# Performance work log

Measured on AMD Instinct MI355X. Metric: run time of the kernel, lower is better.

Reference implementation:

```python
import jax, jax.numpy as jnp
import numpy as np

T, B, N, D, H = 128, 64, 24, 256, 8
F = D // H  # 32


def setup_inputs() -> dict:
    key = jax.random.key(0)
    ks = jax.random.split(key, 7)
    s = 1.0 / np.sqrt(D)  # torch nn.Linear default init range
    inputs = jax.random.normal(ks[0], (T, B, N * D), dtype=jnp.float32)
    Wk = jax.random.uniform(ks[1], (H, F, D), minval=-s, maxval=s, dtype=jnp.float32)
    bk = jax.random.uniform(ks[2], (H, F), minval=-s, maxval=s, dtype=jnp.float32)
    Wv = jax.random.uniform(ks[3], (H, F, D), minval=-s, maxval=s, dtype=jnp.float32)
    bv = jax.random.uniform(ks[4], (H, F), minval=-s, maxval=s, dtype=jnp.float32)
    Wq = jax.random.uniform(ks[5], (H, N, F, D), minval=-s, maxval=s, dtype=jnp.float32)
    bq = jax.random.uniform(ks[6], (H, N, F), minval=-s, maxval=s, dtype=jnp.float32)
    return {"inputs": inputs, "Wk": Wk, "bk": bk, "Wv": Wv, "bv": bv, "Wq": Wq, "bq": bq}


def reference(inputs, Wk, bk, Wv, bv, Wq, bq):
    # inputs: (T, B, N*D) -> (T, B, N, D)
    x = inputs.reshape(T, B, N, D)
    # shared K/V per head: (T, B, H, N, F)
    k = jnp.einsum('tbnd,hfd->tbhnf', x, Wk) + bk[:, None, :]
    v = jnp.einsum('tbnd,hfd->tbhnf', x, Wv) + bv[:, None, :]
    # per-joint Q: joint n uses its own (F, D) weight -> (T, B, H, N, F)
    q = jnp.einsum('tbnd,hnfd->tbhnf', x, Wq) + bq
    # attention over joints, scaled by sqrt(F)
    scores = jnp.einsum('tbhnf,tbhmf->tbhnm', q, k) / jnp.sqrt(jnp.float32(F))
    attn = jax.nn.softmax(scores, axis=-1)
    out = jnp.einsum('tbhnm,tbhmf->tbhnf', attn, v)
    # concat heads along feature dim per joint, then flatten joints: (T, B, N*H*F)
    out = out.transpose(0, 1, 3, 2, 4).reshape(T, B, N * H * F)
    # dropout is identity in eval mode
    return out
```

## Files before the change

kernel.cpp:

```cpp
#include <hip/hip_runtime.h>
#include <hip/hip_bf16.h>
#include <cstdio>

#define TB  8192
#define N_  24
#define D_  256
#define H_  8
#define F_  32
#define ND  6144
#define HNF 6144

typedef unsigned short u16;
typedef __attribute__((ext_vector_type(8))) _Float16 f16x8;
typedef __attribute__((ext_vector_type(8))) short bf16x8;
typedef __attribute__((ext_vector_type(4))) float f32x4;

__device__ __forceinline__ u16 f2b(float f) {
    unsigned int u = __float_as_uint(f);
    return (u16)((u + 0x7FFFu + ((u >> 16) & 1u)) >> 16);
}
__device__ __forceinline__ float b2f(u16 s) {
    return __uint_as_float(((unsigned int)s) << 16);
}
__device__ __forceinline__ u16 f2h(float f) {
    _Float16 h = (_Float16)f;
    u16 u; __builtin_memcpy(&u, &h, 2); return u;
}

__device__ __forceinline__ void gl_lds16(const void* g, void* l) {
    __builtin_amdgcn_global_load_lds(
        (const __attribute__((address_space(1))) unsigned int*)g,
        (__attribute__((address_space(3))) unsigned int*)l, 16, 0, 0);
}

__global__ __launch_bounds__(256) void prep_weights(
    const float* __restrict__ Wk, const float* __restrict__ Wv,
    const float* __restrict__ Wq, u16* __restrict__ Bp)
{
    const int idx = blockIdx.x * 256 + threadIdx.x;
    if (idx >= 24 * 8 * 48 * 64) return;
    const int fr = idx & 15;
    const int fq = (idx >> 4) & 3;
    const int g  = (idx >> 6) % 48;
    const int kt = (idx / (64 * 48)) % 8;
    const int n  = idx / (64 * 48 * 8);
    const int col = g * 16 + fr;
    const int d0  = kt * 32 + fq * 8;
    const int c   = col & 255;
    const float* src;
    if (col < 256)      src = Wk + (size_t)c * 256 + d0;
    else if (col < 512) src = Wv + (size_t)c * 256 + d0;
    else {
        const int h = c >> 5, f = c & 31;
        src = Wq + ((size_t)(h * 24 + n) * 32 + f) * 256 + d0;
    }
    __align__(16) u16 out[8];
    #pragma unroll
    for (int j = 0; j < 8; ++j) out[j] = f2h(src[j]);
    *reinterpret_cast<uint4*>(Bp + (size_t)idx * 8) =
        *reinterpret_cast<const uint4*>(out);
}

__global__ __launch_bounds__(256) void prep_bias(
    const float* __restrict__ bk, const float* __restrict__ bv,
    const float* __restrict__ bq, float* __restrict__ biasp)
{
    const int idx = blockIdx.x * 256 + threadIdx.x;
    if (idx >= 24 * 768) return;
    const int col = idx % 768, n = idx / 768;
    const int c = col & 255;
    float v;
    if (col < 256)      v = bk[c];
    else if (col < 512) v = bv[c];
    else { const int h = c >> 5, f = c & 31; v = bq[(h * 24 + n) * 32 + f]; }
    biasp[n * 768 + col] = v;
}

__global__ __launch_bounds__(512, 4) void proj_mfma(
    const float* __restrict__ x,
    const u16* __restrict__ Bp,
    const float* __restrict__ biasp,
    u16* __restrict__ kb, u16* __restrict__ vb, u16* __restrict__ qb)
{
    const int lin  = blockIdx.x;
    const int mblk = lin & 63;
    const int ct   = (lin >> 6) % 3;
    const int n    = lin / 192;
    const int tb0  = mblk * 128;
    const int tid  = threadIdx.x;
    const int w    = tid >> 6;
    const int lane = tid & 63;
    const int wm   = w >> 2;
    const int wn   = w & 3;
    const int fr   = lane & 15, fq = lane >> 4;

    __shared__ __align__(16) u16 smem[32768];
    char* Ab = (char*)smem;
    char* Bb = (char*)smem + 16384;

    const int arow0 = w * 16 + (lane >> 3);
    const int aclog = (lane & 7) ^ ((lane >> 3) & 7);
    const char* asrc0 = (const char*)x +
        (size_t)(tb0 + arow0) * (ND * 4) + n * 1024 + aclog * 16;

    const char* bsrc0 = (const char*)Bp +
        ((size_t)(n * 8) * 48 + ct * 16 + w * 2) * 1024 + (size_t)lane * 16;

    f32x4 acc[4][4];
    #pragma unroll
    for (int m = 0; m < 4; ++m)
        #pragma unroll
        for (int j = 0; j < 4; ++j) acc[m][j] = (f32x4){0.f, 0.f, 0.f, 0.f};

    for (int kt = 0; kt < 8; ++kt) {
        #pragma unroll
        for (int q = 0; q < 2; ++q) {
            gl_lds16(asrc0 + (size_t)q * (8 * ND * 4) + kt * 128,
                     Ab + (w * 2 + q) * 1024);
            gl_lds16(bsrc0 + (size_t)kt * 49152 + q * 1024,
                     Bb + (w * 2 + q) * 1024);
        }
        __syncthreads();

        f16x8 bfr[4];
        #pragma unroll
        for (int j = 0; j < 4; ++j)
            bfr[j] = *reinterpret_cast<const f16x8*>(
                Bb + ((wn * 4 + j) * 64 + fq * 16 + fr) * 16);

        #pragma unroll
        for (int m = 0; m < 4; ++m) {
            const int rowL = wm * 64 + m * 16 + fr;
            const int c0 = (2 * fq) ^ (fr & 7);
            const f32x4 lo = *reinterpret_cast<const f32x4*>(Ab + rowL * 128 + c0 * 16);
            const f32x4 hi = *reinterpret_cast<const f32x4*>(Ab + rowL * 128 + (c0 ^ 1) * 16);
            f16x8 af;
            #pragma unroll
            for (int e = 0; e < 4; ++e) {
                af[e]     = (_Float16)lo[e];
                af[4 + e] = (_Float16)hi[e];
            }
            #pragma unroll
            for (int j = 0; j < 4; ++j)
                acc[m][j] = __builtin_amdgcn_mfma_f32_16x16x32_f16(
                    af, bfr[j], acc[m][j], 0, 0, 0);
        }
        __syncthreads();
    }

    #pragma unroll
    for (int j = 0; j < 4; ++j) {
        const int colL = wn * 64 + j * 16 + fr;
        const float bs = biasp[n * 768 + ct * 256 + colL];
        #pragma unroll
        for (int m = 0; m < 4; ++m)
            #pragma unroll
            for (int r = 0; r < 4; ++r) {
                const int rowL = wm * 64 + m * 16 + fq * 4 + r;
                const int byte = (rowL * 512 + colL * 2) ^ ((rowL & 7) << 4);
                *reinterpret_cast<u16*>((char*)smem + byte) = f2b(acc[m][j][r] + bs);
            }
    }
    __syncthreads();

    u16* dst = (ct == 0) ? kb : (ct == 1) ? vb : qb;
    #pragma unroll
    for (int it = 0; it < 8; ++it) {
        const int id  = it * 512 + tid;
        const int row = id >> 5;
        const int c   = id & 31;
        const uint4 v = *reinterpret_cast<const uint4*>(
            (char*)smem + (row * 512 + ((c * 16) ^ ((row & 7) << 4))));
        const int cc = c * 8;
        const int h  = cc >> 5, f0 = cc & 31;
        *reinterpret_cast<uint4*>(
            &dst[(size_t)(tb0 + row) * HNF + h * 768 + n * 32 + f0]) = v;
    }
}

__device__ __forceinline__ int swz(int row, int chunk) {
    return row * 32 + (((chunk ^ ((row >> 1) ^ (row >> 3))) & 3) << 3);
}

__global__ __launch_bounds__(256) void attn_mfma(
    const u16* __restrict__ kb,
    const u16* __restrict__ vb,
    const u16* __restrict__ qb,
    float* __restrict__ out)
{
    const int tid  = threadIdx.x;
    const int wid  = tid >> 6;
    const int lane = tid & 63;
    const int fr   = lane & 15;
    const int fq   = lane >> 4;
    const size_t tb = (size_t)blockIdx.x * 4 + wid;

    __shared__ __align__(16) u16 lds[4][2048];
    u16* Pw = lds[wid];
    u16* Vt = lds[wid] + 1024;

    #pragma unroll
    for (int i = 0; i < 4; ++i)
        reinterpret_cast<uint4*>(lds[wid])[lane + i * 64] = (uint4){0, 0, 0, 0};

    const u16* qt = qb + tb * HNF;
    const u16* kt = kb + tb * HNF;
    const u16* vt = vb + tb * HNF;
    float* outp = out + tb * ND;

    const float scale = 0.17677669529663687f;
    const bool colok = fr < 8;

    for (int h = 0; h < H_; ++h) {
        const u16* qh = qt + h * 768;
        const u16* kh = kt + h * 768;
        const u16* vh = vt + h * 768;

        bf16x8 qa[2], ka[2];
        #pragma unroll
        for (int t = 0; t < 2; ++t) {
            int rq = t * 16 + fr; rq = rq < 24 ? rq : 23;
            qa[t] = *reinterpret_cast<const bf16x8*>(qh + rq * 32 + fq * 8);
            ka[t] = *reinterpret_cast<const bf16x8*>(kh + rq * 32 + fq * 8);
        }

        {
            const int m = lane >> 2, q = lane & 3;
            const uint4 vv = *reinterpret_cast<const uint4*>(vh + m * 32 + q * 8);
            #pragma unroll
            for (int j = 0; j < 8; ++j) {
                const int f = q * 8 + j;
                Vt[swz(f, m >> 3) + (m & 7)] = reinterpret_cast<const u16*>(&vv)[j];
            }
            if (lane < 32) {
                const int m2 = 16 + (lane >> 2), q2 = lane & 3;
                const uint4 v2 = *reinterpret_cast<const uint4*>(vh + m2 * 32 + q2 * 8);
                #pragma unroll
                for (int j = 0; j < 8; ++j) {
                    const int f = q2 * 8 + j;
                    Vt[swz(f, m2 >> 3) + (m2 & 7)] = reinterpret_cast<const u16*>(&v2)[j];
                }
            }
        }

        f32x4 S[2][2];
        #pragma unroll
        for (int a = 0; a < 2; ++a)
            #pragma unroll
            for (int b = 0; b < 2; ++b)
                S[a][b] = __builtin_amdgcn_mfma_f32_16x16x32_bf16(
                    qa[a], ka[b], (f32x4){0.f, 0.f, 0.f, 0.f}, 0, 0, 0);

        float inv[2][4];
        #pragma unroll
        for (int t = 0; t < 2; ++t) {
            float e0[4], e1[4];
            #pragma unroll
            for (int r = 0; r < 4; ++r) {
                const float a = S[t][0][r] * scale;
                const float b = colok ? S[t][1][r] * scale : -1e30f;
                float mx = fmaxf(a, b);
                #pragma unroll
                for (int off = 1; off < 16; off <<= 1)
                    mx = fmaxf(mx, __shfl_xor(mx, off));
                e0[r] = __expf(a - mx);
                e1[r] = colok ? __expf(b - mx) : 0.f;
                float sm = e0[r] + e1[r];
                #pragma unroll
                for (int off = 1; off < 16; off <<= 1)
                    sm += __shfl_xor(sm, off);
                inv[t][r] = 1.f / sm;
            }
            #pragma unroll
            for (int r = 0; r < 4; ++r) {
                const int row = t * 16 + fq * 4 + r;
                if (row < 24) {
                    Pw[swz(row, fr >> 3) + (fr & 7)] = f2b(e0[r]);
                    if (colok) {
                        const int c1 = 16 + fr;
                        Pw[swz(row, c1 >> 3) + (c1 & 7)] = f2b(e1[r]);
                    }
                }
            }
        }

        bf16x8 pa[2], vbf[2];
        #pragma unroll
        for (int t = 0; t < 2; ++t)
            pa[t] = *reinterpret_cast<const bf16x8*>(&Pw[swz(t * 16 + fr, fq)]);
        #pragma unroll
        for (int t = 0; t < 2; ++t)
            vbf[t] = *reinterpret_cast<const bf16x8*>(&Vt[swz(t * 16 + fr, fq)]);

        f32x4 O[2][2];
        #pragma unroll
        for (int a = 0; a < 2; ++a)
            #pragma unroll
            for (int b = 0; b < 2; ++b)
                O[a][b] = __builtin_amdgcn_mfma_f32_16x16x32_bf16(
                    pa[a], vbf[b], (f32x4){0.f, 0.f, 0.f, 0.f}, 0, 0, 0);

        #pragma unroll
        for (int a = 0; a < 2; ++a)
            #pragma unroll
            for (int r = 0; r < 4; ++r) {
                const int row = a * 16 + fq * 4 + r;
                if (row < 24) {
                    outp[row * D_ + h * F_ + fr]      = O[a][0][r] * inv[a][r];
                    outp[row * D_ + h * F_ + 16 + fr] = O[a][1][r] * inv[a][r];
                }
            }
    }
}

extern "C" void kernel_launch(void* const* d_in, const int* in_sizes, int n_in,
                              void* d_out, int out_size, void* d_ws, size_t ws_size,
                              hipStream_t stream) {
    const float* x  = (const float*)d_in[0];
    const float* Wk = (const float*)d_in[1];
    const float* bk = (const float*)d_in[2];
    const float* Wv = (const float*)d_in[3];
    const float* bv = (const float*)d_in[4];
    const float* Wq = (const float*)d_in[5];
    const float* bq = (const float*)d_in[6];
    float* out = (float*)d_out;

    const size_t qkv_elems = (size_t)TB * HNF;
    const size_t need = qkv_elems * 2ull * 3ull;
    if (ws_size < need) fprintf(stderr, "ws too small: %zu < %zu\n", ws_size, need);
    u16* kbuf = (u16*)d_ws;
    u16* vbuf = kbuf + qkv_elems;
    u16* qbuf = vbuf + qkv_elems;

    u16*   Bp    = (u16*)d_out;
    float* biasp = (float*)((char*)d_out + (size_t)24 * 8 * 48 * 512 * 2);

    prep_weights<<<2304, 256, 0, stream>>>(Wk, Wv, Wq, Bp);
    prep_bias<<<(24 * 768 + 255) / 256, 256, 0, stream>>>(bk, bv, bq, biasp);
    proj_mfma<<<4608, 512, 0, stream>>>(x, Bp, biasp, kbuf, vbuf, qbuf);
    attn_mfma<<<TB / 4, 256, 0, stream>>>(kbuf, vbuf, qbuf, out);
}
```

Measured before the change: 337.1 us.

## Double-buffer projection GEMM with register-staged fp16 A tiles and prefetch

Restructures the QKV projection GEMM main loop into a double-buffered software pipeline. The A tile (fp32 input) is now loaded into registers, converted to fp16 once per element and written to a swizzled LDS buffer, replacing the repeated fp32 LDS reads and per-wave conversions. B tiles are prefetched into the alternate LDS buffer with async global-to-LDS loads, and the barriers use manual waitcnt with s_setprio around the MFMA block. This aims to overlap global loads with compute and halve the LDS traffic for A, at the cost of more registers and fragile hand-tuned wait counts.

```diff
diff --git a/kernel.cpp b/kernel.cpp
--- a/kernel.cpp
+++ b/kernel.cpp
@@ -95,16 +95,15 @@
     const int fr   = lane & 15, fq = lane >> 4;
 
     __shared__ __align__(16) u16 smem[32768];
-    char* Ab = (char*)smem;
-    char* Bb = (char*)smem + 16384;
-
-    const int arow0 = w * 16 + (lane >> 3);
-    const int aclog = (lane & 7) ^ ((lane >> 3) & 7);
-    const char* asrc0 = (const char*)x +
-        (size_t)(tb0 + arow0) * (ND * 4) + n * 1024 + aclog * 16;
-
-    const char* bsrc0 = (const char*)Bp +
-        ((size_t)(n * 8) * 48 + ct * 16 + w * 2) * 1024 + (size_t)lane * 16;
+    char* const Ab = (char*)smem;
+    char* const Bb = (char*)smem + 16384;
+
+    const int arow = tid >> 2;
+    const int ac   = tid & 3;
+    const float* xsrc = x + (size_t)(tb0 + arow) * ND + n * 256 + ac * 8;
+    const int awbyte = arow * 64 + ((ac ^ ((arow >> 1) & 3)) << 4);
+
+    const size_t bbase = (size_t)(n * 8 * 48 + ct * 16 + w * 2) * 1024 + lane * 16;
 
     f32x4 acc[4][4];
     #pragma unroll
@@ -112,41 +111,88 @@
         #pragma unroll
         for (int j = 0; j < 4; ++j) acc[m][j] = (f32x4){0.f, 0.f, 0.f, 0.f};
 
+    float4 axr[2][2];
+
+    axr[0][0] = *reinterpret_cast<const float4*>(xsrc);
+    axr[0][1] = *reinterpret_cast<const float4*>(xsrc + 4);
+    gl_lds16((const char*)Bp + bbase,        Bb + (w * 2) * 1024);
+    gl_lds16((const char*)Bp + bbase + 1024, Bb + (w * 2 + 1) * 1024);
+    asm volatile("s_waitcnt vmcnt(2)" ::: "memory");
+    {
+        ushort4 hv;
+        hv.x = f2h(axr[0][0].x); hv.y = f2h(axr[0][0].y);
+        hv.z = f2h(axr[0][0].z); hv.w = f2h(axr[0][0].w);
+        ushort4 hv2;
+        hv2.x = f2h(axr[0][1].x); hv2.y = f2h(axr[0][1].y);
+        hv2.z = f2h(axr[0][1].z); hv2.w = f2h(axr[0][1].w);
+        *reinterpret_cast<ushort4*>(Ab + awbyte)     = hv;
+        *reinterpret_cast<ushort4*>(Ab + awbyte + 8) = hv2;
+    }
+    axr[1][0] = *reinterpret_cast<const float4*>(xsrc + 32);
+    axr[1][1] = *reinterpret_cast<const float4*>(xsrc + 36);
+    asm volatile("s_waitcnt lgkmcnt(0)" ::: "memory");
+    asm volatile("s_waitcnt vmcnt(2)" ::: "memory");
+    __builtin_amdgcn_s_barrier();
+    asm volatile("" ::: "memory");
+
+    #pragma unroll
     for (int kt = 0; kt < 8; ++kt) {
-        #pragma unroll
-        for (int q = 0; q < 2; ++q) {
-            gl_lds16(asrc0 + (size_t)q * (8 * ND * 4) + kt * 128,
-                     Ab + (w * 2 + q) * 1024);
-            gl_lds16(bsrc0 + (size_t)kt * 49152 + q * 1024,
-                     Bb + (w * 2 + q) * 1024);
-        }
-        __syncthreads();
-
-        f16x8 bfr[4];
+        const int c = kt & 1, o = c ^ 1;
+
+        if (kt < 7) {
+            const size_t bs = bbase + (size_t)(kt + 1) * 48 * 1024;
+            gl_lds16((const char*)Bp + bs,        Bb + o * 16384 + (w * 2) * 1024);
+            gl_lds16((const char*)Bp + bs + 1024, Bb + o * 16384 + (w * 2 + 1) * 1024);
+        }
+
+        f16x8 bfr[4], afr[4];
         #pragma unroll
         for (int j = 0; j < 4; ++j)
             bfr[j] = *reinterpret_cast<const f16x8*>(
-                Bb + ((wn * 4 + j) * 64 + fq * 16 + fr) * 16);
-
+                Bb + c * 16384 + (wn * 4 + j) * 1024 + lane * 16);
         #pragma unroll
         for (int m = 0; m < 4; ++m) {
-            const int rowL = wm * 64 + m * 16 + fr;
-            const int c0 = (2 * fq) ^ (fr & 7);
-            const f32x4 lo = *reinterpret_cast<const f32x4*>(Ab + rowL * 128 + c0 * 16);
-            const f32x4 hi = *reinterpret_cast<const f32x4*>(Ab + rowL * 128 + (c0 ^ 1) * 16);
-            f16x8 af;
-            #pragma unroll
-            for (int e = 0; e < 4; ++e) {
-                af[e]     = (_Float16)lo[e];
-                af[4 + e] = (_Float16)hi[e];
-            }
-            #pragma unroll
-            for (int j = 0; j < 4; ++j)
+            const int row = wm * 64 + m * 16 + fr;
+            afr[m] = *reinterpret_cast<const f16x8*>(
+                Ab + c * 8192 + row * 64 + ((fq ^ ((fr >> 1) & 3)) << 4));
+        }
+        __builtin_amdgcn_s_setprio(1);
+        #pragma unroll
+        for (int j = 0; j < 4; ++j)
+            #pragma unroll
+            for (int m = 0; m < 4; ++m)
                 acc[m][j] = __builtin_amdgcn_mfma_f32_16x16x32_f16(
-                    af, bfr[j], acc[m][j], 0, 0, 0);
-        }
-        __syncthreads();
-    }
+                    afr[m], bfr[j], acc[m][j], 0, 0, 0);
+        __builtin_amdgcn_s_setprio(0);
+
+        if (kt < 7) {
+            asm volatile("s_waitcnt vmcnt(2)" ::: "memory");
+            __builtin_amdgcn_sched_barrier(0);
+            {
+                const float4 lo = axr[(kt + 1) & 1][0];
+                const float4 hi = axr[(kt + 1) & 1][1];
+                ushort4 hv;
+                hv.x = f2h(lo.x); hv.y = f2h(lo.y); hv.z = f2h(lo.z); hv.w = f2h(lo.w);
+                ushort4 hv2;
+                hv2.x = f2h(hi.x); hv2.y = f2h(hi.y); hv2.z = f2h(hi.z); hv2.w = f2h(hi.w);
+                *reinterpret_cast<ushort4*>(Ab + o * 8192 + awbyte)     = hv;
+                *reinterpret_cast<ushort4*>(Ab + o * 8192 + awbyte + 8) = hv2;
+            }
+            if (kt < 6) {
+                axr[kt & 1][0] = *reinterpret_cast<const float4*>(xsrc + (kt + 2) * 32);
+                axr[kt & 1][1] = *reinterpret_cast<const float4*>(xsrc + (kt + 2) * 32 + 4);
+            }
+            asm volatile("s_waitcnt lgkmcnt(0)" ::: "memory");
+            if (kt < 6) {
+                asm volatile("s_waitcnt vmcnt(2)" ::: "memory");
+            } else {
+                asm volatile("s_waitcnt vmcnt(0)" ::: "memory");
+            }
+            __builtin_amdgcn_s_barrier();
+            asm volatile("" ::: "memory");
+        }
+    }
+    __syncthreads();
 
     #pragma unroll
     for (int j = 0; j < 4; ++j) {
@@ -168,10 +214,10 @@
     for (int it = 0; it < 8; ++it) {
         const int id  = it * 512 + tid;
         const int row = id >> 5;
-        const int c   = id & 31;
+        const int cch = id & 31;
         const uint4 v = *reinterpret_cast<const uint4*>(
-            (char*)smem + (row * 512 + ((c * 16) ^ ((row & 7) << 4))));
-        const int cc = c * 8;
+            (char*)smem + (row * 512 + ((cch * 16) ^ ((row & 7) << 4))));
+        const int cc = cch * 8;
         const int h  = cc >> 5, f0 = cc & 31;
         *reinterpret_cast<uint4*>(
             &dst[(size_t)(tb0 + row) * HNF + h * 768 + n * 32 + f0]) = v;
```

Result: faster. 322.1 us (-4.5%).
